# Performance work log

Measured on AMD Instinct MI355X. Metric: run time of the kernel, lower is better.

## Reference

```python
import jax, jax.numpy as jnp
import numpy as np

T, D, F, E, K = 2048, 512, 2048, 8, 2


def setup_inputs() -> dict:
    key = jax.random.key(0)
    ks = jax.random.split(key, 5)
    scaled = lambda k, shape, fan: jax.random.normal(k, shape, jnp.float32) * (fan ** -0.5)
    x = jax.random.normal(ks[0], (T, D), jnp.float32)
    Wg = scaled(ks[1], (D, E), D)          # gate: Linear(D -> E), no bias
    W1 = scaled(ks[2], (E, D, F), D)       # per-expert up proj
    W3 = scaled(ks[3], (E, D, F), D)       # per-expert gate proj (SwiGLU)
    W2 = scaled(ks[4], (E, F, D), F)       # per-expert down proj
    return {"x": x, "Wg": Wg, "W1": W1, "W2": W2, "W3": W3}


def reference(x, Wg, W1, W2, W3):
    # gate logits + top-k routing (topk over raw logits, softmax over the k picked logits,
    # computed in float32 then cast back -- matches the torch source)
    logits = x @ Wg                                   # [T, E]
    topw, sel = jax.lax.top_k(logits, K)              # [T, K] each
    weights = jax.nn.softmax(topw.astype(jnp.float32), axis=-1).astype(x.dtype)
    out = jnp.zeros_like(x)
    # NOTE: the source uses `output[batch_idx] = ...` (assignment, not +=), so later
    # experts OVERWRITE earlier ones for tokens routed to multiple experts.
    # We replicate that exactly with sequential jnp.where overwrites.
    for i in range(E):
        hit = sel == i                                # [T, K]
        mask = hit.any(axis=-1)                       # [T] tokens routed to expert i
        w_i = jnp.sum(jnp.where(hit, weights, 0.0), axis=-1)  # [T] routing weight
        h = jax.nn.silu(x @ W1[i]) * (x @ W3[i])      # [T, F] SwiGLU
        y = h @ W2[i]                                 # [T, D]
        out = jnp.where(mask[:, None], w_i[:, None] * y, out)
    return out
```

## Files before the change

### kernel.cpp

```cpp
#include <hip/hip_runtime.h>
#include <hip/hip_bf16.h>
#include <math.h>

typedef __attribute__((ext_vector_type(8))) short short8;
typedef __attribute__((ext_vector_type(4))) float f32x4;

#define T_TOK 2048
#define D_DIM 512
#define F_DIM 2048
#define E_NUM 8
#define MAXT1 40

__device__ __forceinline__ unsigned short f2bf(float f) {
  union { float f; unsigned u; } c; c.f = f;
  unsigned u = c.u;
  return (unsigned short)((u + 0x7fffu + ((u >> 16) & 1u)) >> 16);
}

__device__ __forceinline__ void gld16(const void* g, void* l) {
  __builtin_amdgcn_global_load_lds((const __attribute__((address_space(1))) int*)g,
                                   (__attribute__((address_space(3))) int*)l, 16, 0, 0);
}

__global__ __launch_bounds__(256) void k_route(const float* __restrict__ xin,
                                               const float* __restrict__ Wg,
                                               int* __restrict__ jbuf,
                                               float* __restrict__ wbuf,
                                               unsigned short* __restrict__ xb) {
  int gid = blockIdx.x * 256 + threadIdx.x;
  int t = gid >> 5, seg = gid & 31;
  const float* xp = xin + (size_t)t * D_DIM + seg * 16;
  unsigned short* xo = xb + (size_t)t * D_DIM + seg * 16;
  float acc[8];
#pragma unroll
  for (int e = 0; e < 8; ++e) acc[e] = 0.f;
#pragma unroll
  for (int i = 0; i < 4; ++i) {
    float4 v = *(const float4*)(xp + i * 4);
    ushort4 o;
    o.x = f2bf(v.x); o.y = f2bf(v.y); o.z = f2bf(v.z); o.w = f2bf(v.w);
    *(ushort4*)(xo + i * 4) = o;
    const float* xs = (const float*)&v;
#pragma unroll
    for (int q = 0; q < 4; ++q) {
      int d = seg * 16 + i * 4 + q;
      const float4* wr = (const float4*)(Wg + (size_t)d * 8);
      float4 w0 = wr[0], w1 = wr[1];
      acc[0] += xs[q] * w0.x; acc[1] += xs[q] * w0.y;
      acc[2] += xs[q] * w0.z; acc[3] += xs[q] * w0.w;
      acc[4] += xs[q] * w1.x; acc[5] += xs[q] * w1.y;
      acc[6] += xs[q] * w1.z; acc[7] += xs[q] * w1.w;
    }
  }
#pragma unroll
  for (int off = 1; off < 32; off <<= 1)
#pragma unroll
    for (int e = 0; e < 8; ++e) acc[e] += __shfl_xor(acc[e], off);
  if (seg == 0) {
    float l0 = -1e30f, l1 = -1e30f; int i0 = 0, i1 = 0;
#pragma unroll
    for (int e = 0; e < 8; ++e) {
      float l = acc[e];
      if (l > l0) { l1 = l0; i1 = i0; l0 = l; i0 = e; }
      else if (l > l1) { l1 = l; i1 = e; }
    }
    int j; float w;
    if (i0 > i1) { j = i0; w = 1.f / (1.f + expf(l1 - l0)); }
    else         { j = i1; w = 1.f / (1.f + expf(l0 - l1)); }
    jbuf[t] = j; wbuf[t] = w;
  }
}

__global__ __launch_bounds__(256) void k_prep2(const float* __restrict__ W1,
                                               const float* __restrict__ W3,
                                               unsigned short* __restrict__ w1f,
                                               unsigned short* __restrict__ w3f,
                                               const int* __restrict__ jbuf,
                                               int* __restrict__ cntp,
                                               int* __restrict__ basep,
                                               int* __restrict__ list,
                                               int* __restrict__ tl1,
                                               int* __restrict__ ntl) {
  __shared__ float4 tile4[2][64 * 32];
  __shared__ int scnt[8], scur[8];
  int bz = blockIdx.x, tid = threadIdx.x;

  if (bz >= 1024) {
    if (tid < 8) scnt[tid] = 0;
    __syncthreads();
    for (int t = tid; t < T_TOK; t += 256) atomicAdd(&scnt[jbuf[t]], 1);
    __syncthreads();
    if (tid == 0) {
      int run = 0;
      for (int e = 0; e < 8; ++e) {
        cntp[e] = scnt[e]; basep[e] = run; scur[e] = run;
        run += scnt[e];
      }
      int n1 = 0, bb = 0;
      for (int e = 0; e < 8; ++e) {
        for (int m = 0; m < scnt[e]; m += 64) tl1[n1++] = (e << 16) | (bb + m);
        bb += scnt[e];
      }
      ntl[0] = n1;
    }
    __syncthreads();
    for (int t = tid; t < T_TOK; t += 256) {
      int j = jbuf[t];
      int p = atomicAdd(&scur[j], 1);
      list[p] = t;
    }
    return;
  }

  int z = bz >> 6, rem = bz & 63;
  const int K = 512, N = 2048;
  int n0 = (rem & 15) * 128, k0 = (rem >> 4) * 128;
  size_t zsz = (size_t)(K / 32) * (N / 16) * 512;
  const float* in; unsigned short* out;
  if (z < 8) { in = W1 + (size_t)z * K * N;       out = w1f + (size_t)z * zsz; }
  else       { in = W3 + (size_t)(z - 8) * K * N; out = w3f + (size_t)(z - 8) * zsz; }

  int lr = tid >> 5, lc = tid & 31;
  int wv = tid >> 6, l = tid & 63;
  int n4l = (l & 15) >> 2, nr = l & 3, kg = (l >> 4) * 8;

  auto loadT = [&](int buf, int kb0) {
#pragma unroll
    for (int it = 0; it < 8; ++it) {
      int row = it * 8 + lr;
      float4 v = *(const float4*)(in + (size_t)(kb0 + row) * N + n0 + lc * 4);
      tile4[buf][row * 32 + ((lc + (row >> 3) * 4) & 31)] = v;
    }
  };
  auto storeT = [&](int buf, int kb0) {
    const float* tf = (const float*)&tile4[buf][0];
#pragma unroll
    for (int q = 0; q < 4; ++q) {
      int fid = wv * 4 + q;
      int nb = fid >> 1, kb = fid & 1;
      int n4 = nb * 4 + n4l;
      short8 o;
#pragma unroll
      for (int j = 0; j < 8; ++j) {
        int k = kb * 32 + kg + j;
        int slot = k * 32 + ((n4 + (k >> 3) * 4) & 31);
        o[j] = (short)f2bf(tf[slot * 4 + nr]);
      }
      unsigned short* op = out + (((size_t)(n0 / 16 + nb) * (K / 32)) + (kb0 / 32 + kb)) * 512 + l * 8;
      *(short8*)op = o;
    }
  };

  loadT(0, k0);
  __syncthreads();
  loadT(1, k0 + 64);
  storeT(0, k0);
  __syncthreads();
  storeT(1, k0 + 64);
}

__global__ __launch_bounds__(256, 2) void k_ffn1w2(const unsigned short* __restrict__ xb,
                                                   const unsigned short* __restrict__ w1f,
                                                   const unsigned short* __restrict__ w3f,
                                                   const float* __restrict__ W2,
                                                   unsigned short* __restrict__ w2f,
                                                   const int* __restrict__ cntp,
                                                   const int* __restrict__ basep,
                                                   const int* __restrict__ list,
                                                   const int* __restrict__ tl1,
                                                   const int* __restrict__ ntl,
                                                   unsigned short* __restrict__ hbuf) {
  __shared__ __align__(16) unsigned short sA[64 * 512];
  int tid = threadIdx.x, wv = tid >> 6, l = tid & 63;

  if (blockIdx.x >= 640) {
    int idx = blockIdx.x - 640;
    int z = idx >> 6, rem = idx & 63;
    const int K = 2048, N = 512;
    int n0 = (rem & 3) * 128, k0 = (rem >> 2) * 128;
    size_t zsz = (size_t)(K / 32) * (N / 16) * 512;
    const float* in = W2 + (size_t)z * K * N;
    unsigned short* out = w2f + (size_t)z * zsz;
    float4* tile4 = (float4*)sA;

    int lr = tid >> 5, lc = tid & 31;
    int n4l = (l & 15) >> 2, nr = l & 3, kg = (l >> 4) * 8;

    auto loadT = [&](int buf, int kb0) {
#pragma unroll
      for (int it = 0; it < 8; ++it) {
        int row = it * 8 + lr;
        float4 v = *(const float4*)(in + (size_t)(kb0 + row) * N + n0 + lc * 4);
        tile4[buf * 2048 + row * 32 + ((lc + (row >> 3) * 4) & 31)] = v;
      }
    };
    auto storeT = [&](int buf, int kb0) {
      const float* tf = (const float*)&tile4[buf * 2048];
#pragma unroll
      for (int q = 0; q < 4; ++q) {
        int fid = wv * 4 + q;
        int nb = fid >> 1, kb = fid & 1;
        int n4 = nb * 4 + n4l;
        short8 o;
#pragma unroll
        for (int j = 0; j < 8; ++j) {
          int k = kb * 32 + kg + j;
          int slot = k * 32 + ((n4 + (k >> 3) * 4) & 31);
          o[j] = (short)f2bf(tf[slot * 4 + nr]);
        }
        unsigned short* op = out + (((size_t)(n0 / 16 + nb) * (K / 32)) + (kb0 / 32 + kb)) * 512 + l * 8;
        *(short8*)op = o;
      }
    };

    loadT(0, k0);
    __syncthreads();
    loadT(1, k0 + 64);
    storeT(0, k0);
    __syncthreads();
    storeT(1, k0 + 64);
    return;
  }

  int L = blockIdx.x;
  int b = (L & 7) * 80 + (L >> 3);
  int x = b % 40, y = b / 40;
  if (x >= ntl[0]) return;
  int pk = tl1[x];
  int e = pk >> 16, g0 = pk & 0xffff;
  int lim = basep[e] + cntp[e];

#pragma unroll
  for (int it = 0; it < 16; ++it) {
    int row = wv * 16 + it;
    int gr = g0 + row; if (gr >= lim) gr = lim - 1;
    int tok = list[gr];
    int slot = (l & 56) | ((l & 7) ^ (row & 7));
    gld16(xb + (size_t)tok * D_DIM + slot * 8, sA + row * 512);
  }

  const unsigned short* b1a = w1f + ((size_t)(e * 128 + y * 8 + wv) * 16) * 512 + l * 8;
  const unsigned short* b3a = w3f + ((size_t)(e * 128 + y * 8 + wv) * 16) * 512 + l * 8;
  const unsigned short* b1b = w1f + ((size_t)(e * 128 + y * 8 + 4 + wv) * 16) * 512 + l * 8;
  const unsigned short* b3b = w3f + ((size_t)(e * 128 + y * 8 + 4 + wv) * 16) * 512 + l * 8;

  short8 P1[4], P3[4], Q1[4], Q3[4], R1[4], R3[4];
  auto loadS = [&](short8* r1, short8* r3,
                   const unsigned short* p1, const unsigned short* p3, int s) {
#pragma unroll
    for (int q = 0; q < 4; ++q) {
      r1[q] = *(const short8*)(p1 + (size_t)(s * 4 + q) * 512);
      r3[q] = *(const short8*)(p3 + (size_t)(s * 4 + q) * 512);
    }
  };

  f32x4 au[4], av[4];
#pragma unroll
  for (int i = 0; i < 4; ++i) {
    au[i] = (f32x4){0.f, 0.f, 0.f, 0.f};
    av[i] = (f32x4){0.f, 0.f, 0.f, 0.f};
  }

  auto quartC = [&](const short8* r1, const short8* r3, int s) {
#pragma unroll
    for (int q = 0; q < 4; ++q) {
      int kf = s * 4 + q;
      short8 a[4];
#pragma unroll
      for (int i = 0; i < 4; ++i) {
        int r = i * 16 + (l & 15);
        int slot = kf * 4 + (l >> 4);
        int swz = (slot & 56) | ((slot & 7) ^ (r & 7));
        a[i] = *(const short8*)(sA + r * 512 + swz * 8);
      }
#pragma unroll
      for (int i = 0; i < 4; ++i) {
        au[i] = __builtin_amdgcn_mfma_f32_16x16x32_bf16(a[i], r1[q], au[i], 0, 0, 0);
        av[i] = __builtin_amdgcn_mfma_f32_16x16x32_bf16(a[i], r3[q], av[i], 0, 0, 0);
      }
    }
  };

  int cloc = l & 15, rb = (l >> 4) * 4;
  auto writeH = [&](int h) {
    int col = (y * 8 + h * 4 + wv) * 16 + cloc;
#pragma unroll
    for (int i = 0; i < 4; ++i) {
#pragma unroll
      for (int r = 0; r < 4; ++r) {
        int gr = g0 + i * 16 + rb + r;
        if (gr < lim) {
          float uu = au[i][r], vv = av[i][r];
          float hh = (uu / (1.f + expf(-uu))) * vv;
          hbuf[(size_t)gr * F_DIM + col] = f2bf(hh);
        }
      }
      au[i] = (f32x4){0.f, 0.f, 0.f, 0.f};
      av[i] = (f32x4){0.f, 0.f, 0.f, 0.f};
    }
  };

  loadS(P1, P3, b1a, b3a, 0);
  loadS(Q1, Q3, b1a, b3a, 1);
  __syncthreads();
  loadS(R1, R3, b1a, b3a, 2);
  quartC(P1, P3, 0);
  loadS(P1, P3, b1a, b3a, 3);
  quartC(Q1, Q3, 1);
  loadS(Q1, Q3, b1b, b3b, 0);
  quartC(R1, R3, 2);
  loadS(R1, R3, b1b, b3b, 1);
  quartC(P1, P3, 3);
  writeH(0);
  loadS(P1, P3, b1b, b3b, 2);
  quartC(Q1, Q3, 0);
  loadS(Q1, Q3, b1b, b3b, 3);
  quartC(R1, R3, 1);
  quartC(P1, P3, 2);
  quartC(Q1, Q3, 3);
  writeH(1);
}

__global__ __launch_bounds__(256, 3) void k_ffn2(const unsigned short* __restrict__ hbuf,
                                                 const unsigned short* __restrict__ w2f,
                                                 const int* __restrict__ cntp,
                                                 const int* __restrict__ basep,
                                                 const int* __restrict__ list,
                                                 const int* __restrict__ tl1,
                                                 const int* __restrict__ ntl,
                                                 const float* __restrict__ wbuf,
                                                 float* __restrict__ out) {
  int L = blockIdx.x;
  int c = L & 7, q = L >> 3;
  int x = c * 5 + (q % 5);
  int nt = q / 5;
  if (x >= ntl[0]) return;
  int pk = tl1[x];
  int e = pk >> 16, g0 = pk & 0xffff;
  int lim = basep[e] + cntp[e];
  __shared__ unsigned short sA[2 * 8192];
  int tid = threadIdx.x, wv = tid >> 6, l = tid & 63;
  int wr = wv >> 1, wc = wv & 1;

  auto stage = [&](int buf, int ck) {
#pragma unroll
    for (int it = 0; it < 4; ++it) {
      int row0 = it * 16 + wv * 4;
      int row = row0 + (l >> 4);
      int gr = g0 + row; if (gr > T_TOK - 1) gr = T_TOK - 1;
      int sl = (l & 8) | ((l & 7) ^ (row & 7));
      gld16(hbuf + (size_t)gr * F_DIM + ck * 128 + sl * 8, sA + buf * 8192 + row0 * 128);
    }
  };

  const unsigned short* b2p = w2f + ((size_t)(e * 32 + nt * 2 + wc) * 64) * 512 + l * 8;

  short8 Ba[4], Bb[4];
  auto loadB = [&](short8* B, int ck) {
#pragma unroll
    for (int kk = 0; kk < 4; ++kk)
      B[kk] = *(const short8*)(b2p + (size_t)(ck * 4 + kk) * 512);
  };

  f32x4 acc[2];
  acc[0] = (f32x4){0.f, 0.f, 0.f, 0.f};
  acc[1] = (f32x4){0.f, 0.f, 0.f, 0.f};

  auto compute = [&](const short8* B, int cur) {
#pragma unroll
    for (int kk = 0; kk < 4; ++kk) {
      short8 a[2];
#pragma unroll
      for (int i = 0; i < 2; ++i) {
        int r = wr * 32 + i * 16 + (l & 15);
        int slot = kk * 4 + (l >> 4);
        int swz = (slot & 8) | ((slot & 7) ^ (r & 7));
        a[i] = *(const short8*)(sA + cur * 8192 + r * 128 + swz * 8);
      }
      acc[0] = __builtin_amdgcn_mfma_f32_16x16x32_bf16(a[0], B[kk], acc[0], 0, 0, 0);
      acc[1] = __builtin_amdgcn_mfma_f32_16x16x32_bf16(a[1], B[kk], acc[1], 0, 0, 0);
    }
  };

  stage(0, 0);
  loadB(Ba, 0);
  __syncthreads();
  int cur = 0;
  for (int ck = 0; ck < 16; ck += 2) {
    stage(cur ^ 1, ck + 1);
    loadB(Bb, ck + 1);
    compute(Ba, cur);
    __syncthreads();
    cur ^= 1;
    if (ck + 2 < 16) {
      stage(cur ^ 1, ck + 2);
      loadB(Ba, ck + 2);
    }
    compute(Bb, cur);
    __syncthreads();
    cur ^= 1;
  }

  int cloc = l & 15, rb = (l >> 4) * 4;
#pragma unroll
  for (int i = 0; i < 2; ++i)
#pragma unroll
    for (int r = 0; r < 4; ++r) {
      int gr = g0 + wr * 32 + i * 16 + rb + r;
      if (gr < lim) {
        int tok = list[gr];
        out[(size_t)tok * D_DIM + nt * 32 + wc * 16 + cloc] = wbuf[tok] * acc[i][r];
      }
    }
}

extern "C" void kernel_launch(void* const* d_in, const int* in_sizes, int n_in,
                              void* d_out, int out_size, void* d_ws, size_t ws_size,
                              hipStream_t stream) {
  const float* x  = (const float*)d_in[0];
  const float* Wg = (const float*)d_in[1];
  const float* W1 = (const float*)d_in[2];
  const float* W2 = (const float*)d_in[3];
  const float* W3 = (const float*)d_in[4];
  float* out = (float*)d_out;
  char* ws = (char*)d_ws;

  int*            jbuf  = (int*)(ws + 0);
  float*          wbuf  = (float*)(ws + 8192);
  int*            cntp  = (int*)(ws + 16384);
  int*            basep = (int*)(ws + 16448);
  int*            list  = (int*)(ws + 16640);
  int*            tl1   = (int*)(ws + 24832);
  int*            ntl   = (int*)(ws + 25600);
  unsigned short* xb    = (unsigned short*)(ws + 32768);
  unsigned short* w1f   = (unsigned short*)(ws + 32768 + 2097152);
  unsigned short* w3f   = (unsigned short*)(ws + 32768 + 2097152 + 16777216);
  unsigned short* w2f   = (unsigned short*)(ws + 32768 + 2097152 + 2 * 16777216);
  unsigned short* hbuf  = (unsigned short*)(ws + 32768 + 2097152 + 3 * 16777216);

  k_route<<<dim3(256), dim3(256), 0, stream>>>(x, Wg, jbuf, wbuf, xb);
  k_prep2<<<dim3(1025), dim3(256), 0, stream>>>(W1, W3, w1f, w3f, jbuf, cntp, basep, list, tl1, ntl);
  k_ffn1w2<<<dim3(1152), dim3(256), 0, stream>>>(xb, w1f, w3f, W2, w2f, cntp, basep, list, tl1, ntl, hbuf);
  k_ffn2<<<dim3(640), dim3(256), 0, stream>>>(hbuf, w2f, cntp, basep, list, tl1, ntl, wbuf, out);
}
```

Baseline: 76.73 us.

## Load ffn2 A operand directly from global, dropping LDS staging and barriers

The down-projection kernel no longer stages the hidden activations through double-buffered shared memory with barriers. Each wave now loads its A fragments straight from global memory into registers and runs a simple unrolled MFMA loop. Occupancy hint is raised from 3 to 4 blocks per CU. This removes LDS traffic and synchronization, but A rows are re-read by the two column waves without sharing, and per-lane 16-byte loads are strided across rows, which can cost global/L2 bandwidth and latency hiding.

Result: slower. 110.4 us (+43.9%).

```diff
diff --git a/kernel.cpp b/kernel.cpp
--- a/kernel.cpp
+++ b/kernel.cpp
@@ -321,7 +321,7 @@
   writeH(1);
 }
 
-__global__ __launch_bounds__(256, 3) void k_ffn2(const unsigned short* __restrict__ hbuf,
+__global__ __launch_bounds__(256, 4) void k_ffn2(const unsigned short* __restrict__ hbuf,
                                                  const unsigned short* __restrict__ w2f,
                                                  const int* __restrict__ cntp,
                                                  const int* __restrict__ basep,
@@ -338,67 +338,27 @@
   int pk = tl1[x];
   int e = pk >> 16, g0 = pk & 0xffff;
   int lim = basep[e] + cntp[e];
-  __shared__ unsigned short sA[2 * 8192];
   int tid = threadIdx.x, wv = tid >> 6, l = tid & 63;
   int wr = wv >> 1, wc = wv & 1;
 
-  auto stage = [&](int buf, int ck) {
-#pragma unroll
-    for (int it = 0; it < 4; ++it) {
-      int row0 = it * 16 + wv * 4;
-      int row = row0 + (l >> 4);
-      int gr = g0 + row; if (gr > T_TOK - 1) gr = T_TOK - 1;
-      int sl = (l & 8) | ((l & 7) ^ (row & 7));
-      gld16(hbuf + (size_t)gr * F_DIM + ck * 128 + sl * 8, sA + buf * 8192 + row0 * 128);
-    }
-  };
-
+  int ra0 = g0 + wr * 32 + (l & 15);      if (ra0 >= lim) ra0 = lim - 1;
+  int ra1 = g0 + wr * 32 + 16 + (l & 15); if (ra1 >= lim) ra1 = lim - 1;
+  int ko = (l >> 4) * 8;
+  const unsigned short* a0p = hbuf + (size_t)ra0 * F_DIM + ko;
+  const unsigned short* a1p = hbuf + (size_t)ra1 * F_DIM + ko;
   const unsigned short* b2p = w2f + ((size_t)(e * 32 + nt * 2 + wc) * 64) * 512 + l * 8;
-
-  short8 Ba[4], Bb[4];
-  auto loadB = [&](short8* B, int ck) {
-#pragma unroll
-    for (int kk = 0; kk < 4; ++kk)
-      B[kk] = *(const short8*)(b2p + (size_t)(ck * 4 + kk) * 512);
-  };
 
   f32x4 acc[2];
   acc[0] = (f32x4){0.f, 0.f, 0.f, 0.f};
   acc[1] = (f32x4){0.f, 0.f, 0.f, 0.f};
 
-  auto compute = [&](const short8* B, int cur) {
-#pragma unroll
-    for (int kk = 0; kk < 4; ++kk) {
-      short8 a[2];
-#pragma unroll
-      for (int i = 0; i < 2; ++i) {
-        int r = wr * 32 + i * 16 + (l & 15);
-        int slot = kk * 4 + (l >> 4);
-        int swz = (slot & 8) | ((slot & 7) ^ (r & 7));
-        a[i] = *(const short8*)(sA + cur * 8192 + r * 128 + swz * 8);
-      }
-      acc[0] = __builtin_amdgcn_mfma_f32_16x16x32_bf16(a[0], B[kk], acc[0], 0, 0, 0);
-      acc[1] = __builtin_amdgcn_mfma_f32_16x16x32_bf16(a[1], B[kk], acc[1], 0, 0, 0);
-    }
-  };
-
-  stage(0, 0);
-  loadB(Ba, 0);
-  __syncthreads();
-  int cur = 0;
-  for (int ck = 0; ck < 16; ck += 2) {
-    stage(cur ^ 1, ck + 1);
-    loadB(Bb, ck + 1);
-    compute(Ba, cur);
-    __syncthreads();
-    cur ^= 1;
-    if (ck + 2 < 16) {
-      stage(cur ^ 1, ck + 2);
-      loadB(Ba, ck + 2);
-    }
-    compute(Bb, cur);
-    __syncthreads();
-    cur ^= 1;
+#pragma unroll 8
+  for (int kf = 0; kf < 64; ++kf) {
+    short8 a0 = *(const short8*)(a0p + kf * 32);
+    short8 a1 = *(const short8*)(a1p + kf * 32);
+    short8 b  = *(const short8*)(b2p + (size_t)kf * 512);
+    acc[0] = __builtin_amdgcn_mfma_f32_16x16x32_bf16(a0, b, acc[0], 0, 0, 0);
+    acc[1] = __builtin_amdgcn_mfma_f32_16x16x32_bf16(a1, b, acc[1], 0, 0, 0);
   }
 
   int cloc = l & 15, rb = (l >> 4) * 4;
```
